# Kernel tuning notes

Measured on AMD Instinct MI355X. Metric: run time of the kernel, lower is better.

The kernel has to match this reference:

```python
import jax, jax.numpy as jnp
import numpy as np

D_MODEL, D_STATE, EXPAND = 1024, 16, 2
D_INNER = EXPAND * D_MODEL
BATCH, SEQ = 4, 4096


def setup_inputs() -> dict:
    key = jax.random.key(0)
    ks = jax.random.split(key, 9)
    s = 0.02
    return {
        "x": jax.random.normal(ks[0], (BATCH, SEQ, D_MODEL), jnp.float32),
        # torch Linear weight [out,in] stored transposed here as [in,out]
        "W_in": jax.random.normal(ks[1], (D_MODEL, 2 * D_INNER), jnp.float32) * s,
        "conv_w": jax.random.normal(ks[2], (D_INNER, 1, 3), jnp.float32) * s,  # depthwise, groups=D_INNER
        "conv_b": jax.random.normal(ks[3], (D_INNER,), jnp.float32) * s,
        "W_B": jax.random.normal(ks[4], (D_INNER, D_STATE), jnp.float32) * s,
        "W_C": jax.random.normal(ks[5], (D_INNER, D_STATE), jnp.float32) * s,
        "A": jax.random.normal(ks[6], (D_STATE,), jnp.float32),
        "D": jnp.ones((D_INNER,), jnp.float32),
        "W_out": jax.random.normal(ks[7], (D_INNER, D_MODEL), jnp.float32) * s,
    }


def reference(x, W_in, conv_w, conv_b, W_B, W_C, A, D, W_out):
    d_inner = conv_w.shape[0]
    # input projection and split into main / residual gate paths
    xr = jnp.einsum("bld,de->ble", x, W_in)  # [B, L, 2*d_inner]
    x_main, res = xr[..., :d_inner], xr[..., d_inner:]
    # depthwise conv1d along seq (kernel 3, pad 1)
    xc = jax.lax.conv_general_dilated(
        x_main.transpose(0, 2, 1), conv_w, (1,), [(1, 1)],
        dimension_numbers=("NCH", "OIH", "NCH"), feature_group_count=d_inner)
    xc = (xc + conv_b[None, :, None]).transpose(0, 2, 1)  # [B, L, d_inner]
    xc = jax.nn.silu(xc)
    # selective-scan inputs
    Bt = jnp.einsum("bli,is->bls", xc, W_B)  # [B, L, d_state]
    Ct = jnp.einsum("bli,is->bls", xc, W_C)
    decay = jnp.exp(-jax.nn.softplus(A))  # exp(A_diag), [d_state]

    def step(state, bc):
        b_t, c_t = bc
        state = state * decay + b_t  # i=0: zeros*decay + B[0] == B[0]
        return state, jnp.sum(state * c_t, axis=-1)  # scalar per batch

    _, ys = jax.lax.scan(step, jnp.zeros_like(Bt[:, 0]),
                         (Bt.transpose(1, 0, 2), Ct.transpose(1, 0, 2)))
    ys = ys.T  # [B, L]
    y = ys[..., None] + xc * D  # broadcast scan output across d_inner
    y = y * jax.nn.silu(res)
    return jnp.einsum("bli,id->bld", y, W_out)
```

## Files before the change

### kernel.cpp

```cpp
#include <hip/hip_runtime.h>


typedef _Float16 half8 __attribute__((ext_vector_type(8)));
typedef float floatx4 __attribute__((ext_vector_type(4)));

#define D_MODEL 1024
#define D_INNER 2048
#define SEQ     4096
#define NBATCH  4
#define NROWS   (NBATCH * SEQ)
#define CHUNK   16
#define NCHUNK  (SEQ / CHUNK)
#define NTASK   (NBATCH * NCHUNK)

__device__ __forceinline__ void async16(_Float16* lds, const _Float16* g) {
    __builtin_amdgcn_global_load_lds((const __attribute__((address_space(1))) void*)g,
                                     (__attribute__((address_space(3))) void*)lds, 16, 0, 0);
}

__device__ __forceinline__ float siluf(float x) {
    return x / (1.f + __expf(-x));
}

__device__ __forceinline__ float decay_of(const float* A, int s) {
    return __expf(-log1pf(__expf(A[s])));
}


__global__ __launch_bounds__(256) void convert_f32_f16(const float* __restrict__ src,
                                                       _Float16* __restrict__ dst) {
    size_t idx = ((size_t)blockIdx.x * 256 + threadIdx.x) * 8;
    float4 a = *(const float4*)(src + idx);
    float4 b = *(const float4*)(src + idx + 4);
    half8 o = {(_Float16)a.x, (_Float16)a.y, (_Float16)a.z, (_Float16)a.w,
               (_Float16)b.x, (_Float16)b.y, (_Float16)b.z, (_Float16)b.w};
    *(half8*)(dst + idx) = o;
}

__global__ __launch_bounds__(256) void transpose_to_f16(const float* __restrict__ src,
                                                        _Float16* __restrict__ dst,
                                                        int K, int N) {
    __shared__ float tile[32][33];
    int n0 = blockIdx.x * 32, k0 = blockIdx.y * 32;
    int x = threadIdx.x, y = threadIdx.y;
#pragma unroll
    for (int r = 0; r < 32; r += 8)
        tile[y + r][x] = src[(size_t)(k0 + y + r) * N + (n0 + x)];
    __syncthreads();
#pragma unroll
    for (int r = 0; r < 32; r += 8)
        dst[(size_t)(n0 + y + r) * K + (k0 + x)] = (_Float16)tile[x][y + r];
}

__global__ __launch_bounds__(256) void convert_wbct(const float* __restrict__ WB,
                                                    const float* __restrict__ WC,
                                                    _Float16* __restrict__ WBCT) {
    int idx = blockIdx.x * 256 + threadIdx.x;
    int n = idx >> 11, k = idx & 2047;
    float v = (n < 16) ? WB[k * 16 + n] : WC[k * 16 + (n - 16)];
    WBCT[idx] = (_Float16)v;
}

template <typename OutT>
__global__ __launch_bounds__(256) void gemm_tn(const _Float16* __restrict__ A,
                                               const _Float16* __restrict__ BT,
                                               OutT* __restrict__ C,
                                               int M, int N, int K) {
    __shared__ __align__(16) _Float16 As[128 * 64];
    __shared__ __align__(16) _Float16 Bs[128 * 64];
    const int tid = threadIdx.x;
    const int wid = tid >> 6, lane = tid & 63;
    const int row0 = blockIdx.y * 128, col0 = blockIdx.x * 128;
    const int wm = (wid & 1) * 64, wn = (wid >> 1) * 64;

    floatx4 acc[4][4] = {};

    const int sr = lane >> 3;
    const int sc = ((lane & 7) ^ sr) * 8;
    const size_t aBase = (size_t)(row0 + wid * 32 + sr) * K + sc;
    const size_t bBase = (size_t)(col0 + wid * 32 + sr) * K + sc;
    _Float16* ldsA = As + wid * 2048;
    _Float16* ldsB = Bs + wid * 2048;

    const int fr = lane & 15, q = lane >> 4;
    const int frq = fr & 7;

    for (int k0 = 0; k0 < K; k0 += 64) {
        __syncthreads();
#pragma unroll
        for (int t = 0; t < 4; t++) {
            async16(ldsA + t * 512, A + aBase + (size_t)(t * 8) * K + k0);
            async16(ldsB + t * 512, BT + bBase + (size_t)(t * 8) * K + k0);
        }
        __syncthreads();
#pragma unroll
        for (int kk = 0; kk < 2; kk++) {
            const int sw = (((kk << 2) + q) ^ frq) * 8;
            half8 af[4], bf[4];
#pragma unroll
            for (int i = 0; i < 4; i++) {
                af[i] = *(const half8*)(As + (wm + i * 16 + fr) * 64 + sw);
                bf[i] = *(const half8*)(Bs + (wn + i * 16 + fr) * 64 + sw);
            }
#pragma unroll
            for (int i = 0; i < 4; i++)
#pragma unroll
                for (int j = 0; j < 4; j++)
                    acc[i][j] = __builtin_amdgcn_mfma_f32_16x16x32_f16(af[i], bf[j], acc[i][j], 0, 0, 0);
        }
    }

    const int er = (lane >> 4) * 4, ec = lane & 15;
#pragma unroll
    for (int i = 0; i < 4; i++)
#pragma unroll
        for (int j = 0; j < 4; j++)
#pragma unroll
            for (int r = 0; r < 4; r++) {
                int row = row0 + wm + i * 16 + er + r;
                int col = col0 + wn + j * 16 + ec;
                C[(size_t)row * N + col] = (OutT)acc[i][j][r];
            }
}

__global__ __launch_bounds__(256) void bc_gemm(const _Float16* __restrict__ A,
                                               const _Float16* __restrict__ BT,
                                               float* __restrict__ C) {
    const int K = D_INNER;
    __shared__ __align__(16) _Float16 As[64 * 64];
    __shared__ __align__(16) _Float16 Bs[32 * 64];
    const int tid = threadIdx.x, wid = tid >> 6, lane = tid & 63;
    const int row0 = blockIdx.x * 64;
    floatx4 acc[2] = {};

    const int srow = lane >> 3;
    const int scol = (lane & 7) * 8;
    const size_t aOff0 = (size_t)(row0 + wid * 16 + srow) * K + scol;
    const size_t aOff1 = aOff0 + (size_t)8 * K;
    const size_t bOff  = (size_t)(wid * 8 + srow) * K + scol;
    _Float16* ldsA = As + wid * 1024;
    _Float16* ldsB = Bs + wid * 512;
    const int fr = lane & 15, fc = (lane >> 4) * 8;

    for (int k0 = 0; k0 < K; k0 += 64) {
        __syncthreads();
        async16(ldsA,       A + aOff0 + k0);
        async16(ldsA + 512, A + aOff1 + k0);
        async16(ldsB,       BT + bOff + k0);
        __syncthreads();
#pragma unroll
        for (int s = 0; s < 2; s++) {
            half8 af = *(const half8*)(As + (wid * 16 + fr) * 64 + s * 32 + fc);
#pragma unroll
            for (int nj = 0; nj < 2; nj++) {
                half8 bf = *(const half8*)(Bs + (nj * 16 + fr) * 64 + s * 32 + fc);
                acc[nj] = __builtin_amdgcn_mfma_f32_16x16x32_f16(af, bf, acc[nj], 0, 0, 0);
            }
        }
    }
    const int er = (lane >> 4) * 4, ec = lane & 15;
#pragma unroll
    for (int nj = 0; nj < 2; nj++)
#pragma unroll
        for (int r = 0; r < 4; r++)
            C[(size_t)(row0 + wid * 16 + er + r) * 32 + nj * 16 + ec] = acc[nj][r];
}

__global__ __launch_bounds__(256) void conv_silu(const _Float16* __restrict__ xr,
                                                 const float* __restrict__ cw,
                                                 const float* __restrict__ cb,
                                                 _Float16* __restrict__ xc) {
    int row = blockIdx.x;
    int l = row & (SEQ - 1);
    int i = threadIdx.x * 8;
    const _Float16* cur = xr + (size_t)row * 4096 + i;
    half8 c8 = *(const half8*)cur;
    half8 p8 = {}, n8 = {};
    if (l > 0)       p8 = *(const half8*)(cur - 4096);
    if (l < SEQ - 1) n8 = *(const half8*)(cur + 4096);
    half8 o;
#pragma unroll
    for (int j = 0; j < 8; j++) {
        int ii = i + j;
        float a = (float)p8[j] * cw[ii * 3] + (float)c8[j] * cw[ii * 3 + 1] +
                  (float)n8[j] * cw[ii * 3 + 2] + cb[ii];
        o[j] = (_Float16)siluf(a);
    }
    *(half8*)(xc + (size_t)row * D_INNER + i) = o;
}


__global__ __launch_bounds__(256) void scan_p1(const float* __restrict__ BtCt,
                                               const float* __restrict__ A,
                                               float* __restrict__ fin) {
    int g = blockIdx.x * 256 + threadIdx.x;
    int task = g >> 4, s = g & 15;
    int b = task >> 8, c = task & (NCHUNK - 1);
    const float decay = decay_of(A, s);
    size_t r = ((size_t)b * SEQ + c * CHUNK) * 32;
    float st = 0.f;
#pragma unroll
    for (int j = 0; j < CHUNK; j++)
        st = st * decay + BtCt[r + (size_t)j * 32 + s];
    fin[task * 16 + s] = st;
}

__global__ __launch_bounds__(64) void scan_p2(const float* __restrict__ fin,
                                              const float* __restrict__ A,
                                              float* __restrict__ carry) {
    int t = threadIdx.x;
    int b = t >> 4, s = t & 15;
    float decay = decay_of(A, s);
    float d16 = decay;
#pragma unroll
    for (int k = 0; k < 4; k++) d16 *= d16;
    float cy = 0.f;
    for (int c = 0; c < NCHUNK; c++) {
        int idx = ((b * NCHUNK) + c) * 16 + s;
        carry[idx] = cy;
        cy = cy * d16 + fin[idx];
    }
}

__global__ __launch_bounds__(256) void scan_p3_fuse(const float* __restrict__ BtCt,
                                                    const float* __restrict__ A,
                                                    const float* __restrict__ carry,
                                                    const float* __restrict__ D,
                                                    const _Float16* __restrict__ xr,
                                                    _Float16* __restrict__ xc) {
    __shared__ float ysl[CHUNK];
    const int task = blockIdx.x;
    const int b = task >> 8, c = task & (NCHUNK - 1);
    const int row0 = b * SEQ + c * CHUNK;
    const int tid = threadIdx.x;

    if (tid < 16) {
        const int s = tid;
        const float decay = decay_of(A, s);
        float st = carry[task * 16 + s];
        size_t r = (size_t)row0 * 32;
#pragma unroll
        for (int j = 0; j < CHUNK; j++) {
            st = st * decay + BtCt[r + s];
            float y = st * BtCt[r + 16 + s];
            y += __shfl_xor(y, 1, 16);
            y += __shfl_xor(y, 2, 16);
            y += __shfl_xor(y, 4, 16);
            y += __shfl_xor(y, 8, 16);
            if (s == 0) ysl[j] = y;
            r += 32;
        }
    }
    __syncthreads();

#pragma unroll
    for (int it = 0; it < 16; it++) {
        int chunk = it * 256 + tid;
        int rl = chunk >> 8;
        int colb = (chunk & 255) * 8;
        size_t row = (size_t)(row0 + rl);
        float yv = ysl[rl];
        half8 x8 = *(const half8*)(xc + row * D_INNER + colb);
        half8 r8 = *(const half8*)(xr + row * 4096 + 2048 + colb);
        float4 d0 = *(const float4*)(D + colb);
        float4 d1 = *(const float4*)(D + colb + 4);
        half8 o;
        float dd[8] = {d0.x, d0.y, d0.z, d0.w, d1.x, d1.y, d1.z, d1.w};
#pragma unroll
        for (int j = 0; j < 8; j++) {
            float y = yv + (float)x8[j] * dd[j];
            o[j] = (_Float16)(y * siluf((float)r8[j]));
        }
        *(half8*)(xc + row * D_INNER + colb) = o;
    }
}

extern "C" void kernel_launch(void* const* d_in, const int* in_sizes, int n_in,
                              void* d_out, int out_size, void* d_ws, size_t ws_size,
                              hipStream_t stream) {
    const float* x      = (const float*)d_in[0];
    const float* W_in   = (const float*)d_in[1];
    const float* conv_w = (const float*)d_in[2];
    const float* conv_b = (const float*)d_in[3];
    const float* W_B    = (const float*)d_in[4];
    const float* W_C    = (const float*)d_in[5];
    const float* A      = (const float*)d_in[6];
    const float* D      = (const float*)d_in[7];
    const float* W_out  = (const float*)d_in[8];
    float* out = (float*)d_out;

    char* ws = (char*)d_ws;
    size_t off = 0;
    auto alloc = [&](size_t bytes) { size_t o = off; off += (bytes + 255) & ~(size_t)255; return o; };
    _Float16* xh    = (_Float16*)(ws + alloc((size_t)NROWS * D_MODEL * 2));
    _Float16* WinT  = (_Float16*)(ws + alloc((size_t)4096 * 1024 * 2));
    _Float16* WoutT = (_Float16*)(ws + alloc((size_t)1024 * 2048 * 2));
    _Float16* WBCT  = (_Float16*)(ws + alloc((size_t)32 * 2048 * 2));
    _Float16* xr    = (_Float16*)(ws + alloc((size_t)NROWS * 4096 * 2));
    _Float16* xc    = (_Float16*)(ws + alloc((size_t)NROWS * D_INNER * 2));
    float*    BtCt  = (float*)(ws + alloc((size_t)NROWS * 32 * 4));
    float*    fin   = (float*)(ws + alloc((size_t)NTASK * 16 * 4));
    float*    carry = (float*)(ws + alloc((size_t)NTASK * 16 * 4));

    convert_f32_f16<<<(NROWS * D_MODEL) / (256 * 8), 256, 0, stream>>>(x, xh);
    transpose_to_f16<<<dim3(4096 / 32, 1024 / 32), dim3(32, 8), 0, stream>>>(W_in, WinT, 1024, 4096);
    transpose_to_f16<<<dim3(1024 / 32, 2048 / 32), dim3(32, 8), 0, stream>>>(W_out, WoutT, 2048, 1024);
    convert_wbct<<<(32 * 2048) / 256, 256, 0, stream>>>(W_B, W_C, WBCT);
    gemm_tn<_Float16><<<dim3(4096 / 128, NROWS / 128), 256, 0, stream>>>(xh, WinT, xr, NROWS, 4096, 1024);
    conv_silu<<<NROWS, 256, 0, stream>>>(xr, conv_w, conv_b, xc);
    bc_gemm<<<NROWS / 64, 256, 0, stream>>>(xc, WBCT, BtCt);
    scan_p1<<<NTASK * 16 / 256, 256, 0, stream>>>(BtCt, A, fin);
    scan_p2<<<1, 64, 0, stream>>>(fin, A, carry);
    scan_p3_fuse<<<NTASK, 256, 0, stream>>>(BtCt, A, carry, D, xr, xc);
    gemm_tn<float><<<dim3(1024 / 128, NROWS / 128), 256, 0, stream>>>(xc, WoutT, out, NROWS, 1024, 2048);
}
```

Measured before the change: 518.3 us.

## Split-K the B/C projection, chunk the conv kernel, and batch scan loads

The B/C projection GEMM now splits K across two blocks that accumulate into a zeroed buffer with atomics, doubling its grid. The depthwise conv+SiLU kernel now handles 16 rows per block with a sliding window over three input rows, loading the weights once and reading each row once. The scan kernels prefetch B/C values into registers before the serial recurrence and unroll the carry loop. These changes add a zeroing kernel and atomic traffic, and the chunked conv launches far fewer blocks.

After: 508.2 us. Within noise of the previous version (-2.0%).

```diff
diff --git a/kernel.cpp b/kernel.cpp
--- a/kernel.cpp
+++ b/kernel.cpp
@@ -59,6 +59,12 @@
     int n = idx >> 11, k = idx & 2047;
     float v = (n < 16) ? WB[k * 16 + n] : WC[k * 16 + (n - 16)];
     WBCT[idx] = (_Float16)v;
+}
+
+__global__ __launch_bounds__(256) void zero_f32(float* __restrict__ p) {
+    size_t idx = ((size_t)blockIdx.x * 256 + threadIdx.x) * 4;
+    float4 z = {0.f, 0.f, 0.f, 0.f};
+    *(float4*)(p + idx) = z;
 }
 
 template <typename OutT>
@@ -131,6 +137,7 @@
     __shared__ __align__(16) _Float16 Bs[32 * 64];
     const int tid = threadIdx.x, wid = tid >> 6, lane = tid & 63;
     const int row0 = blockIdx.x * 64;
+    const int kbeg = blockIdx.y * (K / 2), kend = kbeg + K / 2;
     floatx4 acc[2] = {};
 
     const int srow = lane >> 3;
@@ -142,7 +149,7 @@
     _Float16* ldsB = Bs + wid * 512;
     const int fr = lane & 15, fc = (lane >> 4) * 8;
 
-    for (int k0 = 0; k0 < K; k0 += 64) {
+    for (int k0 = kbeg; k0 < kend; k0 += 64) {
         __syncthreads();
         async16(ldsA,       A + aOff0 + k0);
         async16(ldsA + 512, A + aOff1 + k0);
@@ -163,30 +170,48 @@
     for (int nj = 0; nj < 2; nj++)
 #pragma unroll
         for (int r = 0; r < 4; r++)
-            C[(size_t)(row0 + wid * 16 + er + r) * 32 + nj * 16 + ec] = acc[nj][r];
-}
-
-__global__ __launch_bounds__(256) void conv_silu(const _Float16* __restrict__ xr,
-                                                 const float* __restrict__ cw,
-                                                 const float* __restrict__ cb,
-                                                 _Float16* __restrict__ xc) {
-    int row = blockIdx.x;
-    int l = row & (SEQ - 1);
-    int i = threadIdx.x * 8;
-    const _Float16* cur = xr + (size_t)row * 4096 + i;
-    half8 c8 = *(const half8*)cur;
-    half8 p8 = {}, n8 = {};
-    if (l > 0)       p8 = *(const half8*)(cur - 4096);
-    if (l < SEQ - 1) n8 = *(const half8*)(cur + 4096);
-    half8 o;
+            atomicAdd(&C[(size_t)(row0 + wid * 16 + er + r) * 32 + nj * 16 + ec], acc[nj][r]);
+}
+
+__global__ __launch_bounds__(256) void conv_silu_chunk(const _Float16* __restrict__ xr,
+                                                       const float* __restrict__ cw,
+                                                       const float* __restrict__ cb,
+                                                       _Float16* __restrict__ xc) {
+    const int task = blockIdx.x;
+    const int c = task & (NCHUNK - 1);
+    const int row0 = (task >> 8) * SEQ + c * CHUNK;
+    const int col0 = threadIdx.x * 8;
+
+    float w0[8], w1[8], w2[8], bb[8];
 #pragma unroll
     for (int j = 0; j < 8; j++) {
-        int ii = i + j;
-        float a = (float)p8[j] * cw[ii * 3] + (float)c8[j] * cw[ii * 3 + 1] +
-                  (float)n8[j] * cw[ii * 3 + 2] + cb[ii];
-        o[j] = (_Float16)siluf(a);
-    }
-    *(half8*)(xc + (size_t)row * D_INNER + i) = o;
+        w0[j] = cw[(col0 + j) * 3];
+        w1[j] = cw[(col0 + j) * 3 + 1];
+        w2[j] = cw[(col0 + j) * 3 + 2];
+        bb[j] = cb[col0 + j];
+    }
+    half8 prev = {}, cur, next;
+    if (c > 0) prev = *(const half8*)(xr + (size_t)(row0 - 1) * 4096 + col0);
+    cur = *(const half8*)(xr + (size_t)row0 * 4096 + col0);
+#pragma unroll
+    for (int r = 0; r < CHUNK; r++) {
+        if (c == NCHUNK - 1 && r == CHUNK - 1) {
+            half8 z = {};
+            next = z;
+        } else {
+            next = *(const half8*)(xr + (size_t)(row0 + r + 1) * 4096 + col0);
+        }
+        half8 o;
+#pragma unroll
+        for (int j = 0; j < 8; j++) {
+            float a = (float)prev[j] * w0[j] + (float)cur[j] * w1[j] +
+                      (float)next[j] * w2[j] + bb[j];
+            o[j] = (_Float16)siluf(a);
+        }
+        *(half8*)(xc + (size_t)(row0 + r) * D_INNER + col0) = o;
+        prev = cur;
+        cur = next;
+    }
 }
 
 
@@ -215,6 +240,7 @@
 #pragma unroll
     for (int k = 0; k < 4; k++) d16 *= d16;
     float cy = 0.f;
+#pragma unroll 8
     for (int c = 0; c < NCHUNK; c++) {
         int idx = ((b * NCHUNK) + c) * 16 + s;
         carry[idx] = cy;
@@ -237,18 +263,28 @@
     if (tid < 16) {
         const int s = tid;
         const float decay = decay_of(A, s);
+        size_t r = (size_t)row0 * 32;
+        float bt[CHUNK], ct[CHUNK];
+#pragma unroll
+        for (int j = 0; j < CHUNK; j++) {
+            bt[j] = BtCt[r + (size_t)j * 32 + s];
+            ct[j] = BtCt[r + (size_t)j * 32 + 16 + s];
+        }
         float st = carry[task * 16 + s];
-        size_t r = (size_t)row0 * 32;
+        float yv[CHUNK];
 #pragma unroll
         for (int j = 0; j < CHUNK; j++) {
-            st = st * decay + BtCt[r + s];
-            float y = st * BtCt[r + 16 + s];
+            st = st * decay + bt[j];
+            yv[j] = st * ct[j];
+        }
+#pragma unroll
+        for (int j = 0; j < CHUNK; j++) {
+            float y = yv[j];
             y += __shfl_xor(y, 1, 16);
             y += __shfl_xor(y, 2, 16);
             y += __shfl_xor(y, 4, 16);
             y += __shfl_xor(y, 8, 16);
             if (s == 0) ysl[j] = y;
-            r += 32;
         }
     }
     __syncthreads();
@@ -306,9 +342,10 @@
     transpose_to_f16<<<dim3(4096 / 32, 1024 / 32), dim3(32, 8), 0, stream>>>(W_in, WinT, 1024, 4096);
     transpose_to_f16<<<dim3(1024 / 32, 2048 / 32), dim3(32, 8), 0, stream>>>(W_out, WoutT, 2048, 1024);
     convert_wbct<<<(32 * 2048) / 256, 256, 0, stream>>>(W_B, W_C, WBCT);
+    zero_f32<<<(NROWS * 32) / (256 * 4), 256, 0, stream>>>(BtCt);
     gemm_tn<_Float16><<<dim3(4096 / 128, NROWS / 128), 256, 0, stream>>>(xh, WinT, xr, NROWS, 4096, 1024);
-    conv_silu<<<NROWS, 256, 0, stream>>>(xr, conv_w, conv_b, xc);
-    bc_gemm<<<NROWS / 64, 256, 0, stream>>>(xc, WBCT, BtCt);
+    conv_silu_chunk<<<NTASK, 256, 0, stream>>>(xr, conv_w, conv_b, xc);
+    bc_gemm<<<dim3(NROWS / 64, 2), 256, 0, stream>>>(xc, WBCT, BtCt);
     scan_p1<<<NTASK * 16 / 256, 256, 0, stream>>>(BtCt, A, fin);
     scan_p2<<<1, 64, 0, stream>>>(fin, A, carry);
     scan_p3_fuse<<<NTASK, 256, 0, stream>>>(BtCt, A, carry, D, xr, xc);
```
